# Kernel optimization log

Measured on AMD Instinct MI355X. Metric: run time of the kernel, lower is better.

Reference implementation:

```python
import jax, jax.numpy as jnp
import numpy as np

D_MODEL = 2048
N_HEADS = 16
N_KV_HEADS = 4
HEAD_DIM = D_MODEL // N_HEADS  # 128
N_REP = N_HEADS // N_KV_HEADS  # 4
ROPE_BASE = 10000.0


def _rope_tables(T, head_dim, dtype):
    inv_freq = 1.0 / (ROPE_BASE ** (jnp.arange(0, head_dim, 2, dtype=jnp.float32) / head_dim))
    t = jnp.arange(T, dtype=jnp.float32)
    freqs = jnp.outer(t, inv_freq)               # [T, hd/2]
    emb = jnp.concatenate([freqs, freqs], axis=-1)  # [T, hd]
    return jnp.cos(emb).astype(dtype), jnp.sin(emb).astype(dtype)


def _rotate_half(x):
    x1, x2 = jnp.split(x, 2, axis=-1)
    return jnp.concatenate([-x2, x1], axis=-1)


def _apply_rope(x, cos, sin):
    # x: [B, H, T, hd]; cos/sin: [T, hd]
    return x * cos[None, None] + _rotate_half(x) * sin[None, None]


def setup_inputs() -> dict:
    key = jax.random.key(0)
    ks = jax.random.split(key, 5)
    B, T = 2, 2048
    s_in = 1.0 / np.sqrt(D_MODEL)
    return {
        "x": jax.random.normal(ks[0], (B, T, D_MODEL), jnp.float32),
        "Wq": jax.random.normal(ks[1], (D_MODEL, D_MODEL), jnp.float32) * s_in,
        "Wk": jax.random.normal(ks[2], (D_MODEL, N_KV_HEADS * HEAD_DIM), jnp.float32) * s_in,
        "Wv": jax.random.normal(ks[3], (D_MODEL, N_KV_HEADS * HEAD_DIM), jnp.float32) * s_in,
        "Wo": jax.random.normal(ks[4], (D_MODEL, D_MODEL), jnp.float32) * s_in,
    }


def reference(x, Wq, Wk, Wv, Wo):
    B, T, C = x.shape
    scale = HEAD_DIM ** -0.5
    q = (x @ Wq).reshape(B, T, N_HEADS, HEAD_DIM).transpose(0, 2, 1, 3)     # [B,H,T,hd]
    k = (x @ Wk).reshape(B, T, N_KV_HEADS, HEAD_DIM).transpose(0, 2, 1, 3)  # [B,Hkv,T,hd]
    v = (x @ Wv).reshape(B, T, N_KV_HEADS, HEAD_DIM).transpose(0, 2, 1, 3)
    cos, sin = _rope_tables(T, HEAD_DIM, x.dtype)
    q = _apply_rope(q, cos, sin)
    k = _apply_rope(k, cos, sin)
    # GQA: group query heads; avoid materializing expanded K/V
    qg = q.reshape(B, N_KV_HEADS, N_REP, T, HEAD_DIM)
    scores = jnp.einsum('bgrtd,bgsd->bgrts', qg, k) * scale                 # [B,Hkv,rep,T,S]
    causal = jnp.tril(jnp.ones((T, T), dtype=bool))
    scores = jnp.where(causal[None, None, None], scores, jnp.finfo(scores.dtype).min)
    attn = jax.nn.softmax(scores, axis=-1)
    out = jnp.einsum('bgrts,bgsd->bgrtd', attn, v)                          # [B,Hkv,rep,T,hd]
    out = out.reshape(B, N_HEADS, T, HEAD_DIM).transpose(0, 2, 1, 3).reshape(B, T, C)
    return out @ Wo, k, v
```

## Files before the change

### kernel.cpp

```cpp
#include <hip/hip_runtime.h>
#include <hip/hip_bf16.h>
#include <type_traits>


typedef short  short8 __attribute__((ext_vector_type(8)));
typedef float  f32x4  __attribute__((ext_vector_type(4)));
typedef float  f32x16 __attribute__((ext_vector_type(16)));

#define AS1(p) ((__attribute__((address_space(1))) void*)(p))
#define AS3(p) ((__attribute__((address_space(3))) void*)(p))

static __device__ inline short bf_bits(float f) {
    __hip_bfloat16 h = __float2bfloat16(f);
    return *reinterpret_cast<short*>(&h);
}

__global__ __launch_bounds__(256) void convert_x_kernel(
    const float* __restrict__ x, __hip_bfloat16* __restrict__ xb)
{
    int i = (blockIdx.x * 256 + threadIdx.x) * 4;
    float4 v = *reinterpret_cast<const float4*>(x + i);
    ushort4 o;
    o.x = (unsigned short)bf_bits(v.x);
    o.y = (unsigned short)bf_bits(v.y);
    o.z = (unsigned short)bf_bits(v.z);
    o.w = (unsigned short)bf_bits(v.w);
    *reinterpret_cast<ushort4*>(reinterpret_cast<unsigned short*>(xb) + i) = o;
}

__global__ void transpose_convert_kernel(
    const float* __restrict__ W, __hip_bfloat16* __restrict__ WT, int K, int N)
{
    __shared__ float tile[32][33];
    int n0 = blockIdx.x * 32, k0 = blockIdx.y * 32;
    int tx = threadIdx.x, ty = threadIdx.y;
#pragma unroll
    for (int i = 0; i < 32; i += 8)
        tile[ty + i][tx] = W[(size_t)(k0 + ty + i) * N + n0 + tx];
    __syncthreads();
#pragma unroll
    for (int i = 0; i < 32; i += 8)
        WT[(size_t)(n0 + ty + i) * K + k0 + tx] = __float2bfloat16(tile[tx][ty + i]);
}

static __device__ inline void xcd_decode(int bid, int M, int N, int& m0, int& n0)
{
    const int xcd = bid & 7;
    const int idx = bid >> 3;
    const int mpx = (M >> 7) >> 3;
    const int rem = idx % (mpx * 4);
    const int mb = xcd * mpx + rem % mpx;
    const int nb = (idx / (mpx * 4)) * 4 + rem / mpx;
    m0 = mb << 7;
    n0 = nb << 7;
}

template <typename CT>
__global__ __launch_bounds__(256) void gemm_bt_kernel(
    const __hip_bfloat16* __restrict__ A,
    const __hip_bfloat16* __restrict__ BT,
    CT* __restrict__ C, int M, int N, int K)
{
    const int tid  = threadIdx.x;
    const int w    = tid >> 6;
    const int lane = tid & 63;
    const int l31  = lane & 31;
    const int hi   = lane >> 5;
    int m0, n0;
    xcd_decode(blockIdx.x, M, N, m0, n0);
    const int wm = (w >> 1) << 6;
    const int wn = (w & 1) << 6;

    __shared__ __hip_bfloat16 As[2][128 * 64];
    __shared__ __hip_bfloat16 Bs[2][128 * 64];

    f32x16 acc[2][2] = {};

#define GSTAGE(buf, k0_)                                                            \
    {                                                                               \
        _Pragma("unroll")                                                           \
        for (int i = 0; i < 4; ++i) {                                               \
            int c = tid + i * 256;                                                  \
            int row = c >> 3;                                                       \
            int soct = (c & 7) ^ (row & 7);                                         \
            const __hip_bfloat16* ga = A  + (size_t)(m0 + row) * K + (k0_) + soct * 8; \
            const __hip_bfloat16* gb = BT + (size_t)(n0 + row) * K + (k0_) + soct * 8; \
            __builtin_amdgcn_global_load_lds(AS1(ga), AS3(&As[buf][c * 8]), 16, 0, 0); \
            __builtin_amdgcn_global_load_lds(AS1(gb), AS3(&Bs[buf][c * 8]), 16, 0, 0); \
        }                                                                           \
    }

    GSTAGE(0, 0);
    __syncthreads();
    int cur = 0;
    const int nk = K >> 6;

    for (int t = 0; t < nk; ++t) {
        if (t + 1 < nk) GSTAGE(cur ^ 1, (t + 1) << 6);

#pragma unroll
        for (int ks = 0; ks < 4; ++ks) {
            const int oct = ((ks * 2 + hi) ^ (l31 & 7)) << 3;
            short8 a[2], b[2];
#pragma unroll
            for (int mi = 0; mi < 2; ++mi)
                a[mi] = *reinterpret_cast<const short8*>(
                    reinterpret_cast<const short*>(&As[cur][0]) + (wm + mi * 32 + l31) * 64 + oct);
#pragma unroll
            for (int ni = 0; ni < 2; ++ni)
                b[ni] = *reinterpret_cast<const short8*>(
                    reinterpret_cast<const short*>(&Bs[cur][0]) + (wn + ni * 32 + l31) * 64 + oct);
#pragma unroll
            for (int mi = 0; mi < 2; ++mi)
#pragma unroll
                for (int ni = 0; ni < 2; ++ni)
                    acc[mi][ni] = __builtin_amdgcn_mfma_f32_32x32x16_bf16(
                        a[mi], b[ni], acc[mi][ni], 0, 0, 0);
        }
        __syncthreads();
        cur ^= 1;
    }
#undef GSTAGE

#pragma unroll
    for (int mi = 0; mi < 2; ++mi)
#pragma unroll
        for (int ni = 0; ni < 2; ++ni)
#pragma unroll
            for (int reg = 0; reg < 16; ++reg) {
                int row = m0 + wm + mi * 32 + (reg & 3) + 8 * (reg >> 2) + 4 * hi;
                int col = n0 + wn + ni * 32 + l31;
                float v = acc[mi][ni][reg];
                if constexpr (std::is_same<CT, float>::value)
                    C[(size_t)row * N + col] = v;
                else
                    C[(size_t)row * N + col] = __float2bfloat16(v);
            }
}

__global__ __launch_bounds__(256) void gemm_qkv_fused(
    const __hip_bfloat16* __restrict__ A,
    const __hip_bfloat16* __restrict__ BT,
    __hip_bfloat16* __restrict__ qkv,
    float* __restrict__ outk,
    float* __restrict__ outv,
    __hip_bfloat16* __restrict__ VT)
{
    const int tid  = threadIdx.x;
    const int w    = tid >> 6;
    const int lane = tid & 63;
    const int l31  = lane & 31;
    const int hi   = lane >> 5;
    int m0, n0;
    xcd_decode(blockIdx.x, 4096, 3072, m0, n0);
    const int wm = w << 5;
    const int K = 2048;

    __shared__ __hip_bfloat16 As[2][128 * 64];
    __shared__ __hip_bfloat16 Bs[2][128 * 64];

    f32x16 acc[4] = {};

#define GSTAGE(buf, k0_)                                                            \
    {                                                                               \
        _Pragma("unroll")                                                           \
        for (int i = 0; i < 4; ++i) {                                               \
            int c = tid + i * 256;                                                  \
            int row = c >> 3;                                                       \
            int soct = (c & 7) ^ (row & 7);                                         \
            const __hip_bfloat16* ga = A  + (size_t)(m0 + row) * K + (k0_) + soct * 8; \
            const __hip_bfloat16* gb = BT + (size_t)(n0 + row) * K + (k0_) + soct * 8; \
            __builtin_amdgcn_global_load_lds(AS1(ga), AS3(&As[buf][c * 8]), 16, 0, 0); \
            __builtin_amdgcn_global_load_lds(AS1(gb), AS3(&Bs[buf][c * 8]), 16, 0, 0); \
        }                                                                           \
    }

    GSTAGE(0, 0);
    __syncthreads();
    int cur = 0;

    for (int t = 0; t < 32; ++t) {
        if (t + 1 < 32) GSTAGE(cur ^ 1, (t + 1) << 6);

#pragma unroll
        for (int ks = 0; ks < 4; ++ks) {
            const int oct = ((ks * 2 + hi) ^ (l31 & 7)) << 3;
            short8 a = *reinterpret_cast<const short8*>(
                reinterpret_cast<const short*>(&As[cur][0]) + (wm + l31) * 64 + oct);
#pragma unroll
            for (int ni = 0; ni < 4; ++ni) {
                short8 b = *reinterpret_cast<const short8*>(
                    reinterpret_cast<const short*>(&Bs[cur][0]) + (ni * 32 + l31) * 64 + oct);
                acc[ni] = __builtin_amdgcn_mfma_f32_32x32x16_bf16(a, b, acc[ni], 0, 0, 0);
            }
        }
        __syncthreads();
        cur ^= 1;
    }
#undef GSTAGE

    const int hc = n0 >> 7;
    if (hc < 20) {
        float invf[2];
#pragma unroll
        for (int ni = 0; ni < 2; ++ni)
            invf[ni] = exp2f((float)(ni * 32 + l31) * -0.20762050593046f);
#pragma unroll
        for (int reg = 0; reg < 16; ++reg) {
            int row = m0 + wm + (reg & 3) + 8 * (reg >> 2) + 4 * hi;
            int b = row >> 11, t = row & 2047;
#pragma unroll
            for (int ni = 0; ni < 2; ++ni) {
                int d = ni * 32 + l31;
                float ang = (float)t * invf[ni];
                float s = __sinf(ang), c = __cosf(ang);
                float x1 = acc[ni][reg], x2 = acc[ni + 2][reg];
                float o1 = x1 * c - x2 * s;
                float o2 = x2 * c + x1 * s;
                __hip_bfloat16* q = qkv + (size_t)row * 3072 + hc * 128 + d;
                q[0]  = __float2bfloat16(o1);
                q[64] = __float2bfloat16(o2);
                if (hc >= 16) {
                    int kh = hc - 16;
                    float* ok = outk + (size_t)((b * 4 + kh) * 2048 + t) * 128 + d;
                    ok[0]  = o1;
                    ok[64] = o2;
                }
            }
        }
    } else {
        const int kh = hc - 20;
#pragma unroll
        for (int reg = 0; reg < 16; ++reg) {
            int row = m0 + wm + (reg & 3) + 8 * (reg >> 2) + 4 * hi;
            int b = row >> 11, t = row & 2047;
#pragma unroll
            for (int ni = 0; ni < 4; ++ni) {
                int d = ni * 32 + l31;
                float v = acc[ni][reg];
                outv[(size_t)((b * 4 + kh) * 2048 + t) * 128 + d] = v;
                VT[(size_t)((b * 4 + kh) * 128 + d) * 2048 + t] = __float2bfloat16(v);
            }
        }
    }
}

__global__ __launch_bounds__(256, 2) void attn_kernel(
    const __hip_bfloat16* __restrict__ qkv,
    const __hip_bfloat16* __restrict__ VT,
    __hip_bfloat16* __restrict__ outO)
{
    const int bh = blockIdx.x;
    const int b = bh >> 4, h = bh & 15;
    const int kh = h >> 2;
    const int yb = blockIdx.y;
    const int qblk = (yb < 8) ? (15 - yb) : (yb - 8);
    const int tid = threadIdx.x;
    const int w = tid >> 6;
    const int lane = tid & 63;
    const int lo16 = lane & 15, grp = lane >> 4;
    const int qrow0 = qblk * 128 + w * 32;

    __shared__ short Ks[2][64 * 128];
    __shared__ short Vs[2][128 * 64];
    __shared__ short Ps[4][32 * 64];

    const short* qkvs = reinterpret_cast<const short*>(qkv);
    const size_t kbase = (size_t)b * 2048 * 3072 + 2048 + kh * 128;
    const short* vtb = reinterpret_cast<const short*>(VT) + (size_t)(b * 4 + kh) * 128 * 2048;
    short* pw = &Ps[w][0];

    short8 qf[2][4];
#pragma unroll
    for (int mi = 0; mi < 2; ++mi) {
        const short* qp = qkvs + (size_t)(b * 2048 + qrow0 + mi * 16 + lo16) * 3072
                        + h * 128 + grp * 8;
#pragma unroll
        for (int ss = 0; ss < 4; ++ss)
            qf[mi][ss] = *reinterpret_cast<const short8*>(qp + ss * 32);
    }

    f32x4 o[2][8] = {};
    f32x4 lac[2] = {};

    short8 ones;
#pragma unroll
    for (int jj = 0; jj < 8; ++jj) ones[jj] = (short)0x3F80;

    const float scl2 = 0.12752749545902973f;
    const int ntiles = qblk * 2 + 2;

#define STAGE(buf, kb_)                                                              \
    {                                                                                \
        _Pragma("unroll")                                                            \
        for (int i = 0; i < 4; ++i) {                                                \
            int c = tid + i * 256;                                                   \
            int row = c >> 4, c16 = (c & 15) ^ (row & 7);                            \
            const short* src = qkvs + kbase + (size_t)((kb_) + row) * 3072 + c16 * 8;\
            __builtin_amdgcn_global_load_lds(AS1(src),                               \
                AS3(&Ks[buf][(w * 64 + i * 256) * 8]), 16, 0, 0);                    \
        }                                                                            \
        _Pragma("unroll")                                                            \
        for (int i = 0; i < 4; ++i) {                                                \
            int c = tid + i * 256;                                                   \
            int d = c >> 3, c8 = (c & 7) ^ (d & 7);                                  \
            const short* src = vtb + (size_t)d * 2048 + (kb_) + c8 * 8;              \
            __builtin_amdgcn_global_load_lds(AS1(src),                               \
                AS3(&Vs[buf][(w * 64 + i * 256) * 8]), 16, 0, 0);                    \
        }                                                                            \
    }

    STAGE(0, 0);
    __syncthreads();
    int cur = 0;

    for (int t = 0; t < ntiles; ++t) {
        const int kb = t * 64;
        if (t + 1 < ntiles) STAGE(cur ^ 1, kb + 64);

        f32x4 sg[2][4];
        __builtin_amdgcn_s_setprio(1);
#pragma unroll
        for (int kg = 0; kg < 4; ++kg) {
            f32x4 a0 = {}, a1 = {};
#pragma unroll
            for (int ss = 0; ss < 4; ++ss) {
                short8 kf = *reinterpret_cast<const short8*>(
                    &Ks[cur][(kg * 16 + lo16) * 128 + (((ss * 4 + grp) ^ (lo16 & 7)) << 3)]);
                a0 = __builtin_amdgcn_mfma_f32_16x16x32_bf16(qf[0][ss], kf, a0, 0, 0, 0);
                a1 = __builtin_amdgcn_mfma_f32_16x16x32_bf16(qf[1][ss], kf, a1, 0, 0, 0);
            }
            sg[0][kg] = a0; sg[1][kg] = a1;
        }
        __builtin_amdgcn_s_setprio(0);

        if (kb + 63 > qrow0) {
#pragma unroll
            for (int mi = 0; mi < 2; ++mi)
#pragma unroll
                for (int kg = 0; kg < 4; ++kg) {
                    const int key = kb + kg * 16 + lo16;
#pragma unroll
                    for (int r = 0; r < 4; ++r) {
                        float v = sg[mi][kg][r] * scl2;
                        sg[mi][kg][r] = (key <= qrow0 + mi * 16 + grp * 4 + r) ? v : -1e30f;
                    }
                }
        } else {
#pragma unroll
            for (int mi = 0; mi < 2; ++mi)
#pragma unroll
                for (int kg = 0; kg < 4; ++kg)
#pragma unroll
                    for (int r = 0; r < 4; ++r) sg[mi][kg][r] *= scl2;
        }

#pragma unroll
        for (int mi = 0; mi < 2; ++mi)
#pragma unroll
            for (int kg = 0; kg < 4; ++kg)
#pragma unroll
                for (int r = 0; r < 4; ++r) {
                    float p = __builtin_amdgcn_exp2f(sg[mi][kg][r]);
                    int row = mi * 16 + grp * 4 + r;
                    int idx = row * 64 + (((kg * 2 + (lo16 >> 3)) ^ (row & 7)) << 3) + (lo16 & 7);
                    pw[idx] = bf_bits(p);
                }

        __builtin_amdgcn_s_setprio(1);
#pragma unroll
        for (int ks = 0; ks < 2; ++ks) {
            short8 pf0 = *reinterpret_cast<const short8*>(
                &pw[(0 * 16 + lo16) * 64 + (((ks * 4 + grp) ^ (lo16 & 7)) << 3)]);
            short8 pf1 = *reinterpret_cast<const short8*>(
                &pw[(1 * 16 + lo16) * 64 + (((ks * 4 + grp) ^ (lo16 & 7)) << 3)]);
            lac[0] = __builtin_amdgcn_mfma_f32_16x16x32_bf16(pf0, ones, lac[0], 0, 0, 0);
            lac[1] = __builtin_amdgcn_mfma_f32_16x16x32_bf16(pf1, ones, lac[1], 0, 0, 0);
#pragma unroll
            for (int jj = 0; jj < 8; ++jj) {
                short8 vf = *reinterpret_cast<const short8*>(
                    &Vs[cur][(jj * 16 + lo16) * 64 + (((ks * 4 + grp) ^ (lo16 & 7)) << 3)]);
                o[0][jj] = __builtin_amdgcn_mfma_f32_16x16x32_bf16(pf0, vf, o[0][jj], 0, 0, 0);
                o[1][jj] = __builtin_amdgcn_mfma_f32_16x16x32_bf16(pf1, vf, o[1][jj], 0, 0, 0);
            }
        }
        __builtin_amdgcn_s_setprio(0);

        __syncthreads();
        cur ^= 1;
    }
#undef STAGE

#pragma unroll
    for (int mi = 0; mi < 2; ++mi)
#pragma unroll
        for (int r = 0; r < 4; ++r) {
            float inv = 1.0f / lac[mi][r];
#pragma unroll
            for (int jj = 0; jj < 8; ++jj) {
                outO[(size_t)(b * 2048 + qrow0 + mi * 16 + grp * 4 + r) * 2048
                     + h * 128 + jj * 16 + lo16] = __float2bfloat16(o[mi][jj][r] * inv);
            }
        }
}

extern "C" void kernel_launch(void* const* d_in, const int* in_sizes, int n_in,
                              void* d_out, int out_size, void* d_ws, size_t ws_size,
                              hipStream_t stream)
{
    (void)in_sizes; (void)n_in; (void)out_size; (void)ws_size;
    const float* x  = (const float*)d_in[0];
    const float* Wq = (const float*)d_in[1];
    const float* Wk = (const float*)d_in[2];
    const float* Wv = (const float*)d_in[3];
    const float* Wo = (const float*)d_in[4];

    float* out0 = (float*)d_out;
    float* outk = out0 + 8388608;
    float* outv = out0 + 10485760;

    __hip_bfloat16* wsb    = (__hip_bfloat16*)d_ws;
    __hip_bfloat16* xb     = wsb;
    __hip_bfloat16* WqkvT  = xb + 8388608;
    __hip_bfloat16* WoT    = WqkvT + 6291456;
    __hip_bfloat16* qkv    = WoT + 4194304;
    __hip_bfloat16* VT     = qkv + 12582912;
    __hip_bfloat16* attn_o = xb;

    convert_x_kernel<<<8192, 256, 0, stream>>>(x, xb);
    transpose_convert_kernel<<<dim3(64, 64), dim3(32, 8), 0, stream>>>(Wq, WqkvT, 2048, 2048);
    transpose_convert_kernel<<<dim3(16, 64), dim3(32, 8), 0, stream>>>(Wk, WqkvT + (size_t)2048 * 2048, 2048, 512);
    transpose_convert_kernel<<<dim3(16, 64), dim3(32, 8), 0, stream>>>(Wv, WqkvT + (size_t)2560 * 2048, 2048, 512);
    transpose_convert_kernel<<<dim3(64, 64), dim3(32, 8), 0, stream>>>(Wo, WoT, 2048, 2048);

    gemm_qkv_fused<<<768, 256, 0, stream>>>(xb, WqkvT, qkv, outk, outv, VT);

    attn_kernel<<<dim3(32, 16), 256, 0, stream>>>(qkv, VT, attn_o);

    gemm_bt_kernel<float><<<512, 256, 0, stream>>>(attn_o, WoT, out0, 4096, 2048, 2048);
}
```

Before: 203.2 us.

## Use triple-buffered BK=32 pipeline with vmcnt waits in GEMM kernels

Both GEMM kernels move from a double-buffered K=64 stage to a three-stage ring of K=32 tiles, prefetching two stages ahead. Each step now waits with explicit s_waitcnt vmcnt counts and a single barrier instead of two __syncthreads, so global loads stay in flight across iterations. Shared-memory use drops and the swizzle is reworked for the 32-wide rows. In exchange there are twice as many loop iterations and barriers, and correctness relies on the hand-set vmcnt counts.

```diff
diff --git a/kernel.cpp b/kernel.cpp
--- a/kernel.cpp
+++ b/kernel.cpp
@@ -54,6 +54,9 @@
     m0 = mb << 7;
     n0 = nb << 7;
 }
+
+#define WAITV4 asm volatile("s_waitcnt vmcnt(4)" ::: "memory")
+#define WAITV0 asm volatile("s_waitcnt vmcnt(0)" ::: "memory")
 
 template <typename CT>
 __global__ __launch_bounds__(256) void gemm_bt_kernel(
@@ -71,45 +74,53 @@
     const int wm = (w >> 1) << 6;
     const int wn = (w & 1) << 6;
 
-    __shared__ __hip_bfloat16 As[2][128 * 64];
-    __shared__ __hip_bfloat16 Bs[2][128 * 64];
+    __shared__ __hip_bfloat16 As[3][128 * 32];
+    __shared__ __hip_bfloat16 Bs[3][128 * 32];
 
     f32x16 acc[2][2] = {};
 
-#define GSTAGE(buf, k0_)                                                            \
-    {                                                                               \
-        _Pragma("unroll")                                                           \
-        for (int i = 0; i < 4; ++i) {                                               \
-            int c = tid + i * 256;                                                  \
-            int row = c >> 3;                                                       \
-            int soct = (c & 7) ^ (row & 7);                                         \
+#define GSTAGE(buf, k0_)                                                             \
+    {                                                                                \
+        _Pragma("unroll")                                                            \
+        for (int i = 0; i < 2; ++i) {                                                \
+            int c = tid + i * 256;                                                   \
+            int row = c >> 2;                                                        \
+            int soct = (c & 3) ^ ((row >> 1) & 3);                                   \
             const __hip_bfloat16* ga = A  + (size_t)(m0 + row) * K + (k0_) + soct * 8; \
             const __hip_bfloat16* gb = BT + (size_t)(n0 + row) * K + (k0_) + soct * 8; \
             __builtin_amdgcn_global_load_lds(AS1(ga), AS3(&As[buf][c * 8]), 16, 0, 0); \
             __builtin_amdgcn_global_load_lds(AS1(gb), AS3(&Bs[buf][c * 8]), 16, 0, 0); \
-        }                                                                           \
-    }
-
+        }                                                                            \
+    }
+
+    const int nk = K >> 5;
     GSTAGE(0, 0);
-    __syncthreads();
-    int cur = 0;
-    const int nk = K >> 6;
+    GSTAGE(1, 32);
+    int cur = 0, stg = 2;
 
     for (int t = 0; t < nk; ++t) {
-        if (t + 1 < nk) GSTAGE(cur ^ 1, (t + 1) << 6);
-
-#pragma unroll
-        for (int ks = 0; ks < 4; ++ks) {
-            const int oct = ((ks * 2 + hi) ^ (l31 & 7)) << 3;
+        if (t == nk - 1) { WAITV0; } else { WAITV4; }
+        __builtin_amdgcn_s_barrier();
+        __builtin_amdgcn_sched_barrier(0);
+        if (t + 2 < nk) GSTAGE(stg, (t + 2) << 5);
+
+#pragma unroll
+        for (int ks = 0; ks < 2; ++ks) {
             short8 a[2], b[2];
 #pragma unroll
-            for (int mi = 0; mi < 2; ++mi)
+            for (int mi = 0; mi < 2; ++mi) {
+                int row = wm + mi * 32 + l31;
                 a[mi] = *reinterpret_cast<const short8*>(
-                    reinterpret_cast<const short*>(&As[cur][0]) + (wm + mi * 32 + l31) * 64 + oct);
-#pragma unroll
-            for (int ni = 0; ni < 2; ++ni)
+                    reinterpret_cast<const short*>(&As[cur][0])
+                    + row * 32 + (((ks * 2 + hi) ^ ((row >> 1) & 3)) << 3));
+            }
+#pragma unroll
+            for (int ni = 0; ni < 2; ++ni) {
+                int row = wn + ni * 32 + l31;
                 b[ni] = *reinterpret_cast<const short8*>(
-                    reinterpret_cast<const short*>(&Bs[cur][0]) + (wn + ni * 32 + l31) * 64 + oct);
+                    reinterpret_cast<const short*>(&Bs[cur][0])
+                    + row * 32 + (((ks * 2 + hi) ^ ((row >> 1) & 3)) << 3));
+            }
 #pragma unroll
             for (int mi = 0; mi < 2; ++mi)
 #pragma unroll
@@ -117,8 +128,8 @@
                     acc[mi][ni] = __builtin_amdgcn_mfma_f32_32x32x16_bf16(
                         a[mi], b[ni], acc[mi][ni], 0, 0, 0);
         }
-        __syncthreads();
-        cur ^= 1;
+        cur = (cur == 2) ? 0 : cur + 1;
+        stg = (stg == 2) ? 0 : stg + 1;
     }
 #undef GSTAGE
 
@@ -156,46 +167,53 @@
     const int wm = w << 5;
     const int K = 2048;
 
-    __shared__ __hip_bfloat16 As[2][128 * 64];
-    __shared__ __hip_bfloat16 Bs[2][128 * 64];
+    __shared__ __hip_bfloat16 As[3][128 * 32];
+    __shared__ __hip_bfloat16 Bs[3][128 * 32];
 
     f32x16 acc[4] = {};
 
-#define GSTAGE(buf, k0_)                                                            \
-    {                                                                               \
-        _Pragma("unroll")                                                           \
-        for (int i = 0; i < 4; ++i) {                                               \
-            int c = tid + i * 256;                                                  \
-            int row = c >> 3;                                                       \
-            int soct = (c & 7) ^ (row & 7);                                         \
+#define GSTAGE(buf, k0_)                                                             \
+    {                                                                                \
+        _Pragma("unroll")                                                            \
+        for (int i = 0; i < 2; ++i) {                                                \
+            int c = tid + i * 256;                                                   \
+            int row = c >> 2;                                                        \
+            int soct = (c & 3) ^ ((row >> 1) & 3);                                   \
             const __hip_bfloat16* ga = A  + (size_t)(m0 + row) * K + (k0_) + soct * 8; \
             const __hip_bfloat16* gb = BT + (size_t)(n0 + row) * K + (k0_) + soct * 8; \
             __builtin_amdgcn_global_load_lds(AS1(ga), AS3(&As[buf][c * 8]), 16, 0, 0); \
             __builtin_amdgcn_global_load_lds(AS1(gb), AS3(&Bs[buf][c * 8]), 16, 0, 0); \
-        }                                                                           \
-    }
-
+        }                                                                            \
+    }
+
+    const int nk = 64;
     GSTAGE(0, 0);
-    __syncthreads();
-    int cur = 0;
-
-    for (int t = 0; t < 32; ++t) {
-        if (t + 1 < 32) GSTAGE(cur ^ 1, (t + 1) << 6);
-
-#pragma unroll
-        for (int ks = 0; ks < 4; ++ks) {
-            const int oct = ((ks * 2 + hi) ^ (l31 & 7)) << 3;
+    GSTAGE(1, 32);
+    int cur = 0, stg = 2;
+
+    for (int t = 0; t < nk; ++t) {
+        if (t == nk - 1) { WAITV0; } else { WAITV4; }
+        __builtin_amdgcn_s_barrier();
+        __builtin_amdgcn_sched_barrier(0);
+        if (t + 2 < nk) GSTAGE(stg, (t + 2) << 5);
+
+#pragma unroll
+        for (int ks = 0; ks < 2; ++ks) {
+            int arow = wm + l31;
             short8 a = *reinterpret_cast<const short8*>(
-                reinterpret_cast<const short*>(&As[cur][0]) + (wm + l31) * 64 + oct);
+                reinterpret_cast<const short*>(&As[cur][0])
+                + arow * 32 + (((ks * 2 + hi) ^ ((arow >> 1) & 3)) << 3));
 #pragma unroll
             for (int ni = 0; ni < 4; ++ni) {
+                int brow = ni * 32 + l31;
                 short8 b = *reinterpret_cast<const short8*>(
-                    reinterpret_cast<const short*>(&Bs[cur][0]) + (ni * 32 + l31) * 64 + oct);
+                    reinterpret_cast<const short*>(&Bs[cur][0])
+                    + brow * 32 + (((ks * 2 + hi) ^ ((brow >> 1) & 3)) << 3));
                 acc[ni] = __builtin_amdgcn_mfma_f32_32x32x16_bf16(a, b, acc[ni], 0, 0, 0);
             }
         }
-        __syncthreads();
-        cur ^= 1;
+        cur = (cur == 2) ? 0 : cur + 1;
+        stg = (stg == 2) ? 0 : stg + 1;
     }
 #undef GSTAGE
 
```

Result: no change. 202.7 us (-0.3%).
